# Optimization experiments

Measured on AMD Instinct MI355X. Metric: run time of the kernel, lower is better.

The kernel has to match this reference:

```python
import jax, jax.numpy as jnp
import numpy as np
import math

B, CF, H, W = 2, 64, 256, 256
CH = 32          # 'channel' init arg
KS, DIL, PAD = 3, 2, 2
IMG_H, IMG_W = 512, 512


def _pos_encode(h, w, d_model):
    # Sinusoidal encoding along x and y, interleaved sin/cos -> [2*d_model, h, w]
    div = jnp.exp(jnp.arange(0, d_model, 2, dtype=jnp.float32) * (-math.log(10000.0) / d_model))  # [d/2]
    ax = jnp.arange(w, dtype=jnp.float32)[None, :] * div[:, None]   # [d/2, w]
    ay = jnp.arange(h, dtype=jnp.float32)[None, :] * div[:, None]   # [d/2, h]
    x = jnp.stack([jnp.sin(ax), jnp.cos(ax)], axis=1).reshape(d_model, w)  # even=sin, odd=cos
    y = jnp.stack([jnp.sin(ay), jnp.cos(ay)], axis=1).reshape(d_model, h)
    x = jnp.broadcast_to(x[:, None, :], (d_model, h, w))
    y = jnp.broadcast_to(y[:, :, None], (d_model, h, w))
    return jnp.concatenate([x, y], axis=0)  # [2*d_model, h, w]


def _unfold3x3(x):
    # F.unfold(kernel=3, dilation=2, padding=2, stride=1) -> [B, C, 9, H, W]
    b, c, h, w = x.shape
    xp = jnp.pad(x, ((0, 0), (0, 0), (PAD, PAD), (PAD, PAD)))
    offs = (0, DIL, 2 * DIL)
    patches = [xp[:, :, i:i + h, j:j + w] for i in offs for j in offs]  # row-major kernel order
    return jnp.stack(patches, axis=2)


def setup_inputs() -> dict:
    key = jax.random.key(0)
    k1, k2, k3, k4, k5 = jax.random.split(key, 5)
    return {
        "inp": jax.random.normal(k1, (B, CF, H, W), dtype=jnp.float32),
        "img": jax.random.uniform(k2, (B, 3, IMG_H, IMG_W), dtype=jnp.float32),
        "w_pos": jax.random.normal(k3, (CH, 2 * CH), dtype=jnp.float32) * 0.1,
        "w_img": jax.random.normal(k4, (CH, 3), dtype=jnp.float32) * 0.1,
        "w_comp": jax.random.normal(k5, (CF,), dtype=jnp.float32) * 0.1,
    }


def reference(inp, img, w_pos, w_img, w_comp):
    b, cf, h, w = inp.shape
    # positional embedding -> 1x1 conv (channel matmul)
    pos = _pos_encode(h, w, CH)                                   # [2*CH, H, W]
    pos_embd = jnp.einsum('oc,chw->ohw', w_pos, pos)              # [CH, H, W]
    pos_embd = jnp.broadcast_to(pos_embd[None], (b, CH, h, w))
    # bilinear resize of image to feature resolution, then 1x1 conv
    rimg = jax.image.resize(img, (b, 3, h, w), method='bilinear')
    rimg = jnp.einsum('oc,bchw->bohw', w_img, rimg)               # [B, CH, H, W]
    em = jnp.concatenate([rimg, pos_embd], axis=1)                # [B, 2*CH, H, W]
    # neighborhood similarity score
    un_em = _unfold3x3(em)                                        # [B, 2CH, 9, H, W]
    feature_score = jnp.einsum('bckhw,bchw->bkhw', un_em, em)     # [B, 9, H, W]
    # feature compatibility: 1x1 conv (dot with w_comp) per neighbor, sigmoid
    un_fea = _unfold3x3(inp)                                      # [B, CF, 9, H, W]
    comp_score = jax.nn.sigmoid(jnp.einsum('bckhw,c->bkhw', un_fea, w_comp))
    phi = comp_score * feature_score                              # [B, 9, H, W]
    weighted_fea = jnp.einsum('bckhw,bkhw->bchw', un_fea, phi)    # [B, CF, H, W]
    return weighted_fea
```

## Files before the change

### kernel.cpp

```cpp
#include <hip/hip_runtime.h>
#include <math.h>

namespace {
constexpr int Bn = 2, CF = 64;
constexpr int H = 256, W = 256, HW = H * W;
constexpr int IH = 512, IW = 512;

constexpr int OFF_MT   = 0;
constexpr int OFF_GXX  = OFF_MT + 256 * 256;
constexpr int OFF_GYY  = OFF_GXX + 3 * 256;
constexpr int OFF_G    = OFF_GYY + 3 * 256;
constexpr int OFF_RIMG = OFF_G + 16;
constexpr int OFF_S    = OFF_RIMG + Bn * 3 * HW;
constexpr int OFF_PX   = OFF_RIMG;
constexpr int OFF_PY   = OFF_RIMG + 32 * 256;
}

__global__ __launch_bounds__(256) void pxy_kernel(
    const float* __restrict__ w_pos,
    float* __restrict__ PX, float* __restrict__ PY)
{
  const int t = threadIdx.x;
  const int o = blockIdx.x;
  float s[16], c[16];
#pragma unroll
  for (int i = 0; i < 16; i++) {
    float d = expf((float)(2 * i) * (-0.2878231366242557f));
    float a = (float)t * d;
    s[i] = sinf(a);
    c[i] = cosf(a);
  }
  const float* wr = w_pos + o * 64;
  float ax = 0.f, ay = 0.f;
#pragma unroll
  for (int i = 0; i < 16; i++) {
    ax += wr[2 * i] * s[i] + wr[2 * i + 1] * c[i];
    ay += wr[32 + 2 * i] * s[i] + wr[33 + 2 * i] * c[i];
  }
  PX[o * 256 + t] = ax;
  PY[o * 256 + t] = ay;
}

__global__ __launch_bounds__(256) void gram_kernel(
    const float* __restrict__ PX, const float* __restrict__ PY,
    const float* __restrict__ w_img,
    float* __restrict__ Mt, float* __restrict__ GXX, float* __restrict__ GYY,
    float* __restrict__ G)
{
  const int a = threadIdx.x;
  const int t = blockIdx.x;

  float m = 0.f;
#pragma unroll
  for (int o = 0; o < 32; o++) m += PX[o * 256 + a] * PY[o * 256 + t];
  Mt[t * 256 + a] = m;

  if (t == 0) {
#pragma unroll
    for (int j = 0; j < 3; j++) {
      const int nb = a + 2 * (j - 1);
      float gx = 0.f, gy = 0.f;
      if (nb >= 0 && nb < 256) {
#pragma unroll
        for (int o = 0; o < 32; o++) {
          gx += PX[o * 256 + a] * PX[o * 256 + nb];
          gy += PY[o * 256 + a] * PY[o * 256 + nb];
        }
      }
      GXX[j * 256 + a] = gx;
      GYY[j * 256 + a] = gy;
    }
    if (a < 9) {
      const int i = a / 3, j = a % 3;
      float g = 0.f;
#pragma unroll
      for (int o = 0; o < 32; o++) g += w_img[o * 3 + i] * w_img[o * 3 + j];
      G[a] = g;
    }
  }
}

__device__ __forceinline__ void resize_taps(int p, int n, float w[4], int idx[4])
{
#pragma unroll
  for (int r = 0; r < 4; r++) {
    int q = 2 * p - 1 + r;
    idx[r] = min(max(q, 0), 2 * n - 1);
  }
  if (p == 0)          { w[0] = 0.f;        w[1] = 3.f / 7.f; w[2] = 3.f / 7.f; w[3] = 1.f / 7.f; }
  else if (p == n - 1) { w[0] = 1.f / 7.f;  w[1] = 3.f / 7.f; w[2] = 3.f / 7.f; w[3] = 0.f; }
  else                 { w[0] = 0.125f;     w[1] = 0.375f;    w[2] = 0.375f;    w[3] = 0.125f; }
}

__global__ __launch_bounds__(256) void rimg_kernel(
    const float* __restrict__ img, float* __restrict__ rimg)
{
  const int p = blockIdx.x * 256 + threadIdx.x;
  const int c = blockIdx.y;
  const int b = blockIdx.z;
  const int x = p & (W - 1);
  const int y = p >> 8;

  float wy[4], wx[4];
  int ry[4], rx[4];
  resize_taps(y, H, wy, ry);
  resize_taps(x, W, wx, rx);

  const float* ip = img + ((size_t)(b * 3 + c) * IH) * IW;
  float acc = 0.f;
#pragma unroll
  for (int r = 0; r < 4; r++) {
    const float* rowp = ip + ry[r] * IW;
    float rs = wx[0] * rowp[rx[0]] + wx[1] * rowp[rx[1]] +
               wx[2] * rowp[rx[2]] + wx[3] * rowp[rx[3]];
    acc += wy[r] * rs;
  }
  rimg[((size_t)(b * 3 + c)) * HW + p] = acc;
}

__global__ __launch_bounds__(256) void smap_kernel(
    const float* __restrict__ inp, const float* __restrict__ w_comp,
    float* __restrict__ smap)
{
  __shared__ float red[256];
  const int lane = threadIdx.x & 63;
  const int cg = threadIdx.x >> 6;
  const int p = blockIdx.x * 64 + lane;
  const int b = blockIdx.z;

  const float* ib = inp + (size_t)b * CF * HW + (size_t)cg * 16 * HW + p;
  float a0 = 0.f, a1 = 0.f, a2 = 0.f, a3 = 0.f;
#pragma unroll
  for (int c = 0; c < 16; c += 4) {
    a0 += ib[(size_t)(c + 0) * HW] * w_comp[cg * 16 + c + 0];
    a1 += ib[(size_t)(c + 1) * HW] * w_comp[cg * 16 + c + 1];
    a2 += ib[(size_t)(c + 2) * HW] * w_comp[cg * 16 + c + 2];
    a3 += ib[(size_t)(c + 3) * HW] * w_comp[cg * 16 + c + 3];
  }
  red[threadIdx.x] = (a0 + a1) + (a2 + a3);
  __syncthreads();
  if (threadIdx.x < 64) {
    smap[(size_t)b * HW + blockIdx.x * 64 + threadIdx.x] =
        red[threadIdx.x] + red[threadIdx.x + 64] +
        red[threadIdx.x + 128] + red[threadIdx.x + 192];
  }
}

__global__ __launch_bounds__(256) void phigather_kernel(
    const float* __restrict__ inp, const float* __restrict__ rimg,
    const float* __restrict__ smap, const float* __restrict__ Mt,
    const float* __restrict__ GXX, const float* __restrict__ GYY,
    const float* __restrict__ G, float* __restrict__ out)
{
  const int cg = blockIdx.x;
  const int p = blockIdx.y * 256 + threadIdx.x;
  const int b = blockIdx.z;
  const int x = p & (W - 1);
  const int y = p >> 8;

  const float* rb = rimg + (size_t)b * 3 * HW;
  const float r0 = rb[p], r1 = rb[HW + p], r2 = rb[2 * HW + p];
  const float g0 = G[0], g1 = G[1], g2 = G[2];
  const float g3 = G[3], g4 = G[4], g5 = G[5];
  const float g6 = G[6], g7 = G[7], g8 = G[8];
  const float* sb = smap + (size_t)b * HW;

  float ph[9];
  int nb[9];
#pragma unroll
  for (int k = 0; k < 9; k++) {
    const int ky = k / 3, kx = k % 3;
    const int ny = y + 2 * (ky - 1), nx = x + 2 * (kx - 1);
    const bool valid = ((unsigned)ny < (unsigned)H) & ((unsigned)nx < (unsigned)W);
    const int cy = min(max(ny, 0), H - 1);
    const int cx = min(max(nx, 0), W - 1);
    const int np = cy * W + cx;
    nb[k] = np;

    const float n0 = rb[np], n1 = rb[HW + np], n2 = rb[2 * HW + np];
    float fs = r0 * (g0 * n0 + g1 * n1 + g2 * n2)
             + r1 * (g3 * n0 + g4 * n1 + g5 * n2)
             + r2 * (g6 * n0 + g7 * n1 + g8 * n2);
    fs += GXX[kx * 256 + x] + GYY[ky * 256 + y]
        + Mt[y * 256 + cx] + Mt[cy * 256 + x];

    const float s = sb[np];
    const float cs = 1.f / (1.f + expf(-s));
    ph[k] = valid ? cs * fs : 0.f;
  }

  const float* ib = inp + (size_t)b * CF * HW + (size_t)cg * 16 * HW;
  float* ob = out + (size_t)b * CF * HW + (size_t)cg * 16 * HW;
#pragma unroll 4
  for (int c = 0; c < 16; c++) {
    const float* ic = ib + (size_t)c * HW;
    float acc = ph[0] * ic[nb[0]];
#pragma unroll
    for (int k = 1; k < 9; k++) acc += ph[k] * ic[nb[k]];
    ob[(size_t)c * HW + p] = acc;
  }
}

extern "C" void kernel_launch(void* const* d_in, const int* in_sizes, int n_in,
                              void* d_out, int out_size, void* d_ws, size_t ws_size,
                              hipStream_t stream)
{
  const float* inp    = (const float*)d_in[0];
  const float* img    = (const float*)d_in[1];
  const float* w_pos  = (const float*)d_in[2];
  const float* w_img  = (const float*)d_in[3];
  const float* w_comp = (const float*)d_in[4];
  float* out = (float*)d_out;
  float* ws  = (float*)d_ws;

  float* Mt   = ws + OFF_MT;
  float* GXX  = ws + OFF_GXX;
  float* GYY  = ws + OFF_GYY;
  float* G    = ws + OFF_G;
  float* rimg = ws + OFF_RIMG;
  float* smap = ws + OFF_S;
  float* PX   = ws + OFF_PX;
  float* PY   = ws + OFF_PY;

  hipLaunchKernelGGL(pxy_kernel, dim3(32), dim3(256), 0, stream, w_pos, PX, PY);
  hipLaunchKernelGGL(gram_kernel, dim3(256), dim3(256), 0, stream,
                     PX, PY, w_img, Mt, GXX, GYY, G);

  hipLaunchKernelGGL(rimg_kernel, dim3(HW / 256, 3, Bn), dim3(256), 0, stream,
                     img, rimg);
  hipLaunchKernelGGL(smap_kernel, dim3(HW / 64, 1, Bn), dim3(256), 0, stream,
                     inp, w_comp, smap);

  hipLaunchKernelGGL(phigather_kernel, dim3(CF / 16, HW / 256, Bn), dim3(256), 0, stream,
                     inp, rimg, smap, Mt, GXX, GYY, G, out);
}
```

Measured before the change: 122.5 us.

## Split phi computation from gather and vectorize gather with float4 row loads

Splits the fused phi+gather kernel in two. A separate kernel computes the 9 phi weights once per pixel and writes them to workspace, where before each of the 4 channel-group blocks recomputed them. The gather kernel then handles 4 adjacent pixels per thread with float4 loads of the left, center and right row segments, and the sigmoid moves into a float4-vectorized reduction kernel. This adds a 9xHW phi buffer round-trip through memory and one more launch, in exchange for removing redundant phi work and scattered scalar gathers.

```diff
diff --git a/kernel.cpp b/kernel.cpp
--- a/kernel.cpp
+++ b/kernel.cpp
@@ -12,6 +12,7 @@
 constexpr int OFF_G    = OFF_GYY + 3 * 256;
 constexpr int OFF_RIMG = OFF_G + 16;
 constexpr int OFF_S    = OFF_RIMG + Bn * 3 * HW;
+constexpr int OFF_PHI  = OFF_S + Bn * HW;
 constexpr int OFF_PX   = OFF_RIMG;
 constexpr int OFF_PY   = OFF_RIMG + 32 * 256;
 }
@@ -118,43 +119,54 @@
   rimg[((size_t)(b * 3 + c)) * HW + p] = acc;
 }
 
-__global__ __launch_bounds__(256) void smap_kernel(
+__global__ __launch_bounds__(256) void sigs_kernel(
     const float* __restrict__ inp, const float* __restrict__ w_comp,
-    float* __restrict__ smap)
-{
-  __shared__ float red[256];
+    float* __restrict__ sigs)
+{
+  __shared__ float4 red[256];
   const int lane = threadIdx.x & 63;
   const int cg = threadIdx.x >> 6;
-  const int p = blockIdx.x * 64 + lane;
+  const int p0 = blockIdx.x * 256 + lane * 4;
   const int b = blockIdx.z;
 
-  const float* ib = inp + (size_t)b * CF * HW + (size_t)cg * 16 * HW + p;
-  float a0 = 0.f, a1 = 0.f, a2 = 0.f, a3 = 0.f;
-#pragma unroll
-  for (int c = 0; c < 16; c += 4) {
-    a0 += ib[(size_t)(c + 0) * HW] * w_comp[cg * 16 + c + 0];
-    a1 += ib[(size_t)(c + 1) * HW] * w_comp[cg * 16 + c + 1];
-    a2 += ib[(size_t)(c + 2) * HW] * w_comp[cg * 16 + c + 2];
-    a3 += ib[(size_t)(c + 3) * HW] * w_comp[cg * 16 + c + 3];
-  }
-  red[threadIdx.x] = (a0 + a1) + (a2 + a3);
+  const float* ib = inp + (size_t)b * CF * HW + (size_t)cg * 16 * HW + p0;
+  float4 acc = {0.f, 0.f, 0.f, 0.f};
+#pragma unroll
+  for (int c = 0; c < 16; c++) {
+    const float4 v = *reinterpret_cast<const float4*>(ib + (size_t)c * HW);
+    const float wc = w_comp[cg * 16 + c];
+    acc.x += v.x * wc; acc.y += v.y * wc;
+    acc.z += v.z * wc; acc.w += v.w * wc;
+  }
+  red[threadIdx.x] = acc;
   __syncthreads();
   if (threadIdx.x < 64) {
-    smap[(size_t)b * HW + blockIdx.x * 64 + threadIdx.x] =
-        red[threadIdx.x] + red[threadIdx.x + 64] +
-        red[threadIdx.x + 128] + red[threadIdx.x + 192];
-  }
-}
-
-__global__ __launch_bounds__(256) void phigather_kernel(
-    const float* __restrict__ inp, const float* __restrict__ rimg,
-    const float* __restrict__ smap, const float* __restrict__ Mt,
-    const float* __restrict__ GXX, const float* __restrict__ GYY,
-    const float* __restrict__ G, float* __restrict__ out)
-{
-  const int cg = blockIdx.x;
-  const int p = blockIdx.y * 256 + threadIdx.x;
-  const int b = blockIdx.z;
+    const float4 a = red[threadIdx.x];
+    const float4 b1 = red[threadIdx.x + 64];
+    const float4 c1 = red[threadIdx.x + 128];
+    const float4 d = red[threadIdx.x + 192];
+    float4 s;
+    s.x = (a.x + b1.x) + (c1.x + d.x);
+    s.y = (a.y + b1.y) + (c1.y + d.y);
+    s.z = (a.z + b1.z) + (c1.z + d.z);
+    s.w = (a.w + b1.w) + (c1.w + d.w);
+    s.x = 1.f / (1.f + expf(-s.x));
+    s.y = 1.f / (1.f + expf(-s.y));
+    s.z = 1.f / (1.f + expf(-s.z));
+    s.w = 1.f / (1.f + expf(-s.w));
+    *reinterpret_cast<float4*>(sigs + (size_t)b * HW +
+                               blockIdx.x * 256 + threadIdx.x * 4) = s;
+  }
+}
+
+__global__ __launch_bounds__(256) void phi_kernel(
+    const float* __restrict__ rimg, const float* __restrict__ sigs,
+    const float* __restrict__ Mt, const float* __restrict__ GXX,
+    const float* __restrict__ GYY, const float* __restrict__ G,
+    float* __restrict__ phi)
+{
+  const int p = blockIdx.x * 256 + threadIdx.x;
+  const int b = blockIdx.y;
   const int x = p & (W - 1);
   const int y = p >> 8;
 
@@ -163,10 +175,9 @@
   const float g0 = G[0], g1 = G[1], g2 = G[2];
   const float g3 = G[3], g4 = G[4], g5 = G[5];
   const float g6 = G[6], g7 = G[7], g8 = G[8];
-  const float* sb = smap + (size_t)b * HW;
-
-  float ph[9];
-  int nb[9];
+  const float* sb = sigs + (size_t)b * HW;
+  float* phb = phi + (size_t)b * 9 * HW;
+
 #pragma unroll
   for (int k = 0; k < 9; k++) {
     const int ky = k / 3, kx = k % 3;
@@ -175,7 +186,6 @@
     const int cy = min(max(ny, 0), H - 1);
     const int cx = min(max(nx, 0), W - 1);
     const int np = cy * W + cx;
-    nb[k] = np;
 
     const float n0 = rb[np], n1 = rb[HW + np], n2 = rb[2 * HW + np];
     float fs = r0 * (g0 * n0 + g1 * n1 + g2 * n2)
@@ -184,20 +194,62 @@
     fs += GXX[kx * 256 + x] + GYY[ky * 256 + y]
         + Mt[y * 256 + cx] + Mt[cy * 256 + x];
 
-    const float s = sb[np];
-    const float cs = 1.f / (1.f + expf(-s));
-    ph[k] = valid ? cs * fs : 0.f;
-  }
-
-  const float* ib = inp + (size_t)b * CF * HW + (size_t)cg * 16 * HW;
-  float* ob = out + (size_t)b * CF * HW + (size_t)cg * 16 * HW;
-#pragma unroll 4
-  for (int c = 0; c < 16; c++) {
+    phb[(size_t)k * HW + p] = valid ? sb[np] * fs : 0.f;
+  }
+}
+
+__global__ __launch_bounds__(256) void gather_kernel(
+    const float* __restrict__ inp, const float* __restrict__ phi,
+    float* __restrict__ out)
+{
+  const int tid = threadIdx.x;
+  const int p0 = (blockIdx.y * 256 + tid) * 4;
+  const int b = blockIdx.z;
+  const int c0 = blockIdx.x * 8;
+  const int x0 = p0 & (W - 1);
+  const int y  = p0 >> 8;
+
+  const float* phb = phi + (size_t)b * 9 * HW + p0;
+  float4 ph[9];
+#pragma unroll
+  for (int k = 0; k < 9; k++)
+    ph[k] = *reinterpret_cast<const float4*>(phb + (size_t)k * HW);
+
+  const int xl = max(x0 - 4, 0);
+  const int xr = min(x0 + 4, W - 4);
+  int off[3][3];
+#pragma unroll
+  for (int ky = 0; ky < 3; ky++) {
+    const int cy = min(max(y + 2 * (ky - 1), 0), H - 1);
+    off[ky][0] = cy * W + xl;
+    off[ky][1] = cy * W + x0;
+    off[ky][2] = cy * W + xr;
+  }
+
+  const float* ib = inp + ((size_t)b * CF + c0) * HW;
+  float* ob = out + ((size_t)b * CF + c0) * HW + p0;
+#pragma unroll 2
+  for (int c = 0; c < 8; c++) {
     const float* ic = ib + (size_t)c * HW;
-    float acc = ph[0] * ic[nb[0]];
-#pragma unroll
-    for (int k = 1; k < 9; k++) acc += ph[k] * ic[nb[k]];
-    ob[(size_t)c * HW + p] = acc;
+    float4 acc = {0.f, 0.f, 0.f, 0.f};
+#pragma unroll
+    for (int ky = 0; ky < 3; ky++) {
+      const float4 q0 = *reinterpret_cast<const float4*>(ic + off[ky][0]);
+      const float4 q1 = *reinterpret_cast<const float4*>(ic + off[ky][1]);
+      const float4 q2 = *reinterpret_cast<const float4*>(ic + off[ky][2]);
+      const float a[12] = {q0.x, q0.y, q0.z, q0.w,
+                           q1.x, q1.y, q1.z, q1.w,
+                           q2.x, q2.y, q2.z, q2.w};
+#pragma unroll
+      for (int kx = 0; kx < 3; kx++) {
+        const float4 w = ph[ky * 3 + kx];
+        acc.x += w.x * a[2 + 2 * kx + 0];
+        acc.y += w.y * a[2 + 2 * kx + 1];
+        acc.z += w.z * a[2 + 2 * kx + 2];
+        acc.w += w.w * a[2 + 2 * kx + 3];
+      }
+    }
+    *reinterpret_cast<float4*>(ob + (size_t)c * HW) = acc;
   }
 }
 
@@ -218,7 +270,8 @@
   float* GYY  = ws + OFF_GYY;
   float* G    = ws + OFF_G;
   float* rimg = ws + OFF_RIMG;
-  float* smap = ws + OFF_S;
+  float* sigs = ws + OFF_S;
+  float* phi  = ws + OFF_PHI;
   float* PX   = ws + OFF_PX;
   float* PY   = ws + OFF_PY;
 
@@ -228,9 +281,12 @@
 
   hipLaunchKernelGGL(rimg_kernel, dim3(HW / 256, 3, Bn), dim3(256), 0, stream,
                      img, rimg);
-  hipLaunchKernelGGL(smap_kernel, dim3(HW / 64, 1, Bn), dim3(256), 0, stream,
-                     inp, w_comp, smap);
-
-  hipLaunchKernelGGL(phigather_kernel, dim3(CF / 16, HW / 256, Bn), dim3(256), 0, stream,
-                     inp, rimg, smap, Mt, GXX, GYY, G, out);
-}
+  hipLaunchKernelGGL(sigs_kernel, dim3(HW / 256, 1, Bn), dim3(256), 0, stream,
+                     inp, w_comp, sigs);
+
+  hipLaunchKernelGGL(phi_kernel, dim3(HW / 256, Bn), dim3(256), 0, stream,
+                     rimg, sigs, Mt, GXX, GYY, G, phi);
+
+  hipLaunchKernelGGL(gather_kernel, dim3(CF / 8, HW / 1024, Bn), dim3(256), 0, stream,
+                     inp, phi, out);
+}
```

After: 135.8 us. 1.11x slower.
